# Performance work log

Hardware: AMD Instinct MI355X
Metric: run time of the kernel (lower is better)

The kernel has to match this reference:

```python
import jax, jax.numpy as jnp
import numpy as np

EMBED_DIM = 1024
NUM_HEADS = 16
HEAD_DIM = EMBED_DIM // NUM_HEADS
SCALE = HEAD_DIM ** -0.5


def setup_inputs() -> dict:
    key = jax.random.key(0)
    ks = jax.random.split(key, 9)
    B, N = 2, 2048
    s = EMBED_DIM ** -0.5  # ~ torch Linear init scale
    x = jax.random.normal(ks[0], (B, N, EMBED_DIM), dtype=jnp.float32)
    Wq = jax.random.uniform(ks[1], (EMBED_DIM, EMBED_DIM), jnp.float32, -s, s)
    bq = jax.random.uniform(ks[2], (EMBED_DIM,), jnp.float32, -s, s)
    Wk = jax.random.uniform(ks[3], (EMBED_DIM, EMBED_DIM), jnp.float32, -s, s)
    bk = jax.random.uniform(ks[4], (EMBED_DIM,), jnp.float32, -s, s)
    Wv = jax.random.uniform(ks[5], (EMBED_DIM, EMBED_DIM), jnp.float32, -s, s)
    bv = jax.random.uniform(ks[6], (EMBED_DIM,), jnp.float32, -s, s)
    Wo = jax.random.uniform(ks[7], (EMBED_DIM, EMBED_DIM), jnp.float32, -s, s)
    bo = jax.random.uniform(ks[8], (EMBED_DIM,), jnp.float32, -s, s)
    return {"x": x, "Wq": Wq, "bq": bq, "Wk": Wk, "bk": bk,
            "Wv": Wv, "bv": bv, "Wo": Wo, "bo": bo}


def reference(x, Wq, bq, Wk, bk, Wv, bv, Wo, bo):
    B, N, R = x.shape
    H, D = NUM_HEADS, HEAD_DIM
    # projections: Linear(x) = x @ W^T + b; reshape to (B, H, N, D)
    def proj(W, b):
        return (x @ W.T + b).reshape(B, N, H, D).transpose(0, 2, 1, 3)
    q = proj(Wq, bq)
    k = proj(Wk, bk)
    v = proj(Wv, bv)
    attn = jnp.einsum('bhnd,bhmd->bhnm', q, k) * SCALE  # (B,H,N,N)
    attn = jax.nn.softmax(attn, axis=-1)
    out = jnp.einsum('bhnm,bhmd->bhnd', attn, v)        # (B,H,N,D)
    out = out.transpose(0, 2, 1, 3).reshape(B, N, R)
    return out @ Wo.T + bo
```

## Files before the change

kernel.cpp:

```cpp
#include <hip/hip_runtime.h>
#include <stdint.h>

typedef __bf16 bf16;
typedef __bf16 bf16x4 __attribute__((ext_vector_type(4)));
typedef __bf16 bf16x8 __attribute__((ext_vector_type(8)));
typedef float f32x4 __attribute__((ext_vector_type(4)));

#define MFMA16(a, b, c) __builtin_amdgcn_mfma_f32_16x16x32_bf16((a), (b), (c), 0, 0, 0)

#define EMBED 1024
#define SEQ   2048
#define MROWS 4096
#define ATTN_QSCALE 0.1803368801111f

__device__ __forceinline__ void gl2lds16(const bf16* g, bf16* l) {
    __builtin_amdgcn_global_load_lds(
        (const __attribute__((address_space(1))) void*)g,
        (__attribute__((address_space(3))) void*)l,
        16, 0, 0);
}

__global__ __launch_bounds__(256) void cast_all_kernel(
    const float* __restrict__ x,  const float* __restrict__ Wq,
    const float* __restrict__ Wk, const float* __restrict__ Wv,
    const float* __restrict__ Wo, bf16* __restrict__ dst) {
    const int blk = blockIdx.x;
    const float* src;
    size_t so, dofs;
    if (blk < 2048) {
        src = x; so = (size_t)blk * 2048; dofs = so;
    } else {
        const int w = (blk - 2048) >> 9;
        so  = (size_t)((blk - 2048) & 511) * 2048;
        src = (w == 0) ? Wq : (w == 1) ? Wk : (w == 2) ? Wv : Wo;
        dofs = (size_t)(4 + w) * 1024 * 1024 + so;
    }
    const size_t i = (size_t)threadIdx.x * 8;
    float4 a = *(const float4*)(src + so + i);
    float4 b = *(const float4*)(src + so + i + 4);
    bf16x8 o;
    o[0] = (bf16)a.x; o[1] = (bf16)a.y; o[2] = (bf16)a.z; o[3] = (bf16)a.w;
    o[4] = (bf16)b.x; o[5] = (bf16)b.y; o[6] = (bf16)b.z; o[7] = (bf16)b.w;
    *(bf16x8*)(dst + dofs + i) = o;
}

template <bool SCALE>
__device__ __forceinline__ void gemm_tile(const bf16* __restrict__ A,
                                          const bf16* __restrict__ W,
                                          const float* __restrict__ bias,
                                          bf16* __restrict__ C,
                                          int m0, int n0, bf16* smem) {
    const int lane = threadIdx.x & 63;
    const int wv   = threadIdx.x >> 6;
    const int wm   = (wv >> 1) * 64;
    const int wn   = (wv & 1) * 64;
    const int fr   = lane & 15;
    const int quad = lane >> 4;
    const int srow = wv * 16 + (lane >> 2);
    const int swz  = ((lane & 3) ^ ((lane >> 2) & 3)) * 8;
    const int fcol = (quad ^ (fr & 3)) * 8;

    f32x4 acc[4][4];
#pragma unroll
    for (int mt = 0; mt < 4; ++mt)
#pragma unroll
        for (int nt = 0; nt < 4; ++nt)
            acc[mt][nt] = (f32x4){0.f, 0.f, 0.f, 0.f};

    auto stage = [&](int kt, int bb) {
        bf16* As = smem + bb * 8192;
        bf16* Bs = As + 4096;
        const int k0 = kt * 32;
#pragma unroll
        for (int c = 0; c < 2; ++c) {
            gl2lds16(A + (size_t)(m0 + c * 64 + srow) * 1024 + k0 + swz,
                     &As[(c * 64 + wv * 16) * 32]);
            gl2lds16(W + (size_t)(n0 + c * 64 + srow) * 1024 + k0 + swz,
                     &Bs[(c * 64 + wv * 16) * 32]);
        }
    };

    stage(0, 0);
    stage(1, 1);
#pragma unroll
    for (int kt = 0; kt < 32; ++kt) {
        if (kt < 31) asm volatile("s_waitcnt vmcnt(4)" ::: "memory");
        else         asm volatile("s_waitcnt vmcnt(0)" ::: "memory");
        __builtin_amdgcn_s_barrier();
        if (kt < 30) stage(kt + 2, (kt + 2) % 3);
        const bf16* As = smem + (kt % 3) * 8192;
        const bf16* Bs = As + 4096;
        bf16x8 af[4], bfr[4];
#pragma unroll
        for (int t = 0; t < 4; ++t) {
            af[t]  = *(const bf16x8*)&As[(wm + t * 16 + fr) * 32 + fcol];
            bfr[t] = *(const bf16x8*)&Bs[(wn + t * 16 + fr) * 32 + fcol];
        }
        __builtin_amdgcn_s_setprio(1);
#pragma unroll
        for (int mt = 0; mt < 4; ++mt)
#pragma unroll
            for (int nt = 0; nt < 4; ++nt)
                acc[mt][nt] = MFMA16(af[mt], bfr[nt], acc[mt][nt]);
        __builtin_amdgcn_s_setprio(0);
    }

    float bv[4];
#pragma unroll
    for (int nt = 0; nt < 4; ++nt)
        bv[nt] = bias[n0 + wn + nt * 16 + fr];
    const int row4 = quad * 4;
#pragma unroll
    for (int mt = 0; mt < 4; ++mt)
#pragma unroll
        for (int nt = 0; nt < 4; ++nt)
#pragma unroll
            for (int r = 0; r < 4; ++r) {
                int m = m0 + wm + mt * 16 + row4 + r;
                int n = n0 + wn + nt * 16 + fr;
                float v = acc[mt][nt][r] + bv[nt];
                if (SCALE) v *= ATTN_QSCALE;
                C[(size_t)m * 1024 + n] = (bf16)v;
            }
}

__device__ __forceinline__ void v_tile(const bf16* __restrict__ x,
                                       const bf16* __restrict__ Wv,
                                       const float* __restrict__ bias,
                                       bf16* __restrict__ VT,
                                       int m0, int n0, bf16* smem) {
    const int lane = threadIdx.x & 63;
    const int wv   = threadIdx.x >> 6;
    const int wmW  = (wv >> 1) * 64;
    const int wnT  = (wv & 1) * 64;
    const int f    = lane & 15;
    const int quad = lane >> 4;
    const int srow = wv * 16 + (lane >> 2);
    const int swz  = ((lane & 3) ^ ((lane >> 2) & 3)) * 8;
    const int fcol = (quad ^ (f & 3)) * 8;

    f32x4 acc[4][4];
#pragma unroll
    for (int mt = 0; mt < 4; ++mt)
#pragma unroll
        for (int nt = 0; nt < 4; ++nt)
            acc[mt][nt] = (f32x4){0.f, 0.f, 0.f, 0.f};

    auto stage = [&](int kt, int bb) {
        bf16* As = smem + bb * 8192;
        bf16* Bs = As + 4096;
        const int k0 = kt * 32;
#pragma unroll
        for (int c = 0; c < 2; ++c) {
            gl2lds16(x  + (size_t)(m0 + c * 64 + srow) * 1024 + k0 + swz,
                     &As[(c * 64 + wv * 16) * 32]);
            gl2lds16(Wv + (size_t)(n0 + c * 64 + srow) * 1024 + k0 + swz,
                     &Bs[(c * 64 + wv * 16) * 32]);
        }
    };

    stage(0, 0);
    stage(1, 1);
#pragma unroll
    for (int kt = 0; kt < 32; ++kt) {
        if (kt < 31) asm volatile("s_waitcnt vmcnt(4)" ::: "memory");
        else         asm volatile("s_waitcnt vmcnt(0)" ::: "memory");
        __builtin_amdgcn_s_barrier();
        if (kt < 30) stage(kt + 2, (kt + 2) % 3);
        const bf16* As = smem + (kt % 3) * 8192;
        const bf16* Bs = As + 4096;
        bf16x8 wf[4], xf[4];
#pragma unroll
        for (int t = 0; t < 4; ++t) {
            wf[t] = *(const bf16x8*)&Bs[(wmW + t * 16 + f) * 32 + fcol];
            xf[t] = *(const bf16x8*)&As[(wnT + t * 16 + f) * 32 + fcol];
        }
        __builtin_amdgcn_s_setprio(1);
#pragma unroll
        for (int mt = 0; mt < 4; ++mt)
#pragma unroll
            for (int nt = 0; nt < 4; ++nt)
                acc[mt][nt] = MFMA16(wf[mt], xf[nt], acc[mt][nt]);
        __builtin_amdgcn_s_setprio(0);
    }

    float4 b4[4];
#pragma unroll
    for (int mt = 0; mt < 4; ++mt)
        b4[mt] = *(const float4*)&bias[n0 + wmW + mt * 16 + quad * 4];

    __syncthreads();

#pragma unroll
    for (int mt = 0; mt < 4; ++mt)
#pragma unroll
        for (int nt = 0; nt < 4; ++nt) {
            const int tok = wnT + nt * 16 + f;
#pragma unroll
            for (int r = 0; r < 4; ++r) {
                const float bvr = (r == 0) ? b4[mt].x : (r == 1) ? b4[mt].y
                                : (r == 2) ? b4[mt].z : b4[mt].w;
                smem[(wmW + mt * 16 + quad * 4 + r) * 136 + tok] =
                    (bf16)(acc[mt][nt][r] + bvr);
            }
        }
    __syncthreads();

    const int n_r  = threadIdx.x >> 4;
    const int t8   = (threadIdx.x & 15) * 8;
    const int base = t8 & ~31;
    const int u4   = ((t8 >> 3) & 3) * 4;
    const int bb   = m0 >> 11;
    const int tokg = (m0 & 2047) + t8;
#pragma unroll
    for (int p = 0; p < 8; ++p) {
        const int n_loc = p * 16 + n_r;
        const bf16* row = &smem[n_loc * 136];
        bf16x4 a = *(const bf16x4*)&row[base + u4];
        bf16x4 b = *(const bf16x4*)&row[base + 16 + u4];
        bf16x8 v = {a[0], a[1], a[2], a[3], b[0], b[1], b[2], b[3]};
        *(bf16x8*)&VT[((size_t)(bb * 1024 + n0 + n_loc)) * 2048 + tokg] = v;
    }
}

__global__ __launch_bounds__(256) void qkv_kernel(
    const bf16* __restrict__ x,
    const bf16* __restrict__ Wq, const float* __restrict__ bq,
    const bf16* __restrict__ Wk, const float* __restrict__ bk,
    const bf16* __restrict__ Wv, const float* __restrict__ bv,
    bf16* __restrict__ Q, bf16* __restrict__ K, bf16* __restrict__ VT) {
    __shared__ __align__(16) bf16 smem[24576];
    const int m0    = blockIdx.x * 128;
    const int which = blockIdx.y >> 3;
    const int n0    = (blockIdx.y & 7) * 128;
    if (which == 0)      gemm_tile<true>(x, Wq, bq, Q, m0, n0, smem);
    else if (which == 1) gemm_tile<false>(x, Wk, bk, K, m0, n0, smem);
    else                 v_tile(x, Wv, bv, VT, m0, n0, smem);
}

__global__ __launch_bounds__(256) void oproj_kernel(
    const bf16* __restrict__ A, const bf16* __restrict__ W,
    const float* __restrict__ bias, float* __restrict__ C) {
    const int m0 = blockIdx.x * 128;
    const int n0 = blockIdx.y * 64;

    __shared__ __align__(16) bf16 smem[18432];

    const int lane = threadIdx.x & 63;
    const int wv   = threadIdx.x >> 6;
    const int wm   = (wv >> 1) * 64;
    const int wn   = (wv & 1) * 32;
    const int fr   = lane & 15;
    const int quad = lane >> 4;
    const int srow = wv * 16 + (lane >> 2);
    const int swz  = ((lane & 3) ^ ((lane >> 2) & 3)) * 8;
    const int fcol = (quad ^ (fr & 3)) * 8;

    f32x4 acc[4][2];
#pragma unroll
    for (int mt = 0; mt < 4; ++mt)
#pragma unroll
        for (int nt = 0; nt < 2; ++nt)
            acc[mt][nt] = (f32x4){0.f, 0.f, 0.f, 0.f};

    auto stage = [&](int kt, int bb) {
        bf16* As = smem + bb * 6144;
        bf16* Bs = As + 4096;
        const int k0 = kt * 32;
#pragma unroll
        for (int c = 0; c < 2; ++c)
            gl2lds16(A + (size_t)(m0 + c * 64 + srow) * 1024 + k0 + swz,
                     &As[(c * 64 + wv * 16) * 32]);
        gl2lds16(W + (size_t)(n0 + srow) * 1024 + k0 + swz,
                 &Bs[(wv * 16) * 32]);
    };

    stage(0, 0);
    stage(1, 1);
#pragma unroll
    for (int kt = 0; kt < 32; ++kt) {
        if (kt < 31) asm volatile("s_waitcnt vmcnt(3)" ::: "memory");
        else         asm volatile("s_waitcnt vmcnt(0)" ::: "memory");
        __builtin_amdgcn_s_barrier();
        if (kt < 30) stage(kt + 2, (kt + 2) % 3);
        const bf16* As = smem + (kt % 3) * 6144;
        const bf16* Bs = As + 4096;
        bf16x8 af[4], bfr[2];
#pragma unroll
        for (int t = 0; t < 4; ++t)
            af[t] = *(const bf16x8*)&As[(wm + t * 16 + fr) * 32 + fcol];
#pragma unroll
        for (int t = 0; t < 2; ++t)
            bfr[t] = *(const bf16x8*)&Bs[(wn + t * 16 + fr) * 32 + fcol];
        __builtin_amdgcn_s_setprio(1);
#pragma unroll
        for (int mt = 0; mt < 4; ++mt)
#pragma unroll
            for (int nt = 0; nt < 2; ++nt)
                acc[mt][nt] = MFMA16(af[mt], bfr[nt], acc[mt][nt]);
        __builtin_amdgcn_s_setprio(0);
    }

    float bv[2];
#pragma unroll
    for (int nt = 0; nt < 2; ++nt)
        bv[nt] = bias[n0 + wn + nt * 16 + fr];
    const int row4 = quad * 4;
#pragma unroll
    for (int mt = 0; mt < 4; ++mt)
#pragma unroll
        for (int nt = 0; nt < 2; ++nt)
#pragma unroll
            for (int r = 0; r < 4; ++r) {
                int m = m0 + wm + mt * 16 + row4 + r;
                int n = n0 + wn + nt * 16 + fr;
                C[(size_t)m * 1024 + n] = acc[mt][nt][r] + bv[nt];
            }
}

__global__ __launch_bounds__(256, 2) void attn_kernel(
    const bf16* __restrict__ Q, const bf16* __restrict__ K,
    const bf16* __restrict__ VT, bf16* __restrict__ Opart,
    float* __restrict__ lpart) {
    const int tid  = threadIdx.x;
    const int lane = tid & 63;
    const int wv   = tid >> 6;
    const int quad = lane >> 4;
    const int f    = lane & 15;
    const int lin  = blockIdx.y * 16 + blockIdx.x;
    const int sw   = (lin & 7) * 64 + (lin >> 3);
    const int qh   = sw & 15;
    const int bh   = sw >> 4;
    const int qt   = qh >> 1;
    const int half = qh & 1;
    const int q0   = qt * 256;
    const int kvb  = half * 1024;
    const int b    = bh >> 4;
    const int h    = bh & 15;

    const bf16* Qp = Q + ((size_t)b * SEQ) * 1024 + (size_t)h * 64;
    const bf16* Kp = K + ((size_t)b * SEQ) * 1024 + (size_t)h * 64;
    const bf16* Vp = VT + ((size_t)(b * 1024 + h * 64)) * 2048;
    bf16*  Op = Opart + (size_t)half * MROWS * 1024
                      + ((size_t)b * SEQ) * 1024 + (size_t)h * 64;
    float* lp = lpart + ((size_t)(half * 2 + b) * 16 + h) * SEQ;

    __shared__ bf16 Ks[4][64 * 64];
    __shared__ bf16 VTs[4][64 * 64];

    bf16x8 qf[4][2];
#pragma unroll
    for (int qg = 0; qg < 4; ++qg) {
        const bf16* qrow = Qp + (size_t)(q0 + wv * 64 + qg * 16 + f) * 1024;
        qf[qg][0] = *(const bf16x8*)(qrow + quad * 8);
        qf[qg][1] = *(const bf16x8*)(qrow + 32 + quad * 8);
    }

    const int srow = wv * 8 + (lane >> 3);
    const int swz  = (((lane & 7) ^ ((lane >> 3) & 7))) * 8;
    auto stageK = [&](int t, int bb) {
        const int kv0 = kvb + t * 64;
#pragma unroll
        for (int i = 0; i < 2; ++i)
            gl2lds16(Kp + (size_t)(kv0 + i * 32 + srow) * 1024 + swz,
                     &Ks[bb][(i * 32 + wv * 8) * 64]);
    };
    auto stageVT = [&](int t, int bb) {
        const int kv0 = kvb + t * 64;
#pragma unroll
        for (int i = 0; i < 2; ++i)
            gl2lds16(Vp + (size_t)(i * 32 + srow) * 2048 + kv0 + swz,
                     &VTs[bb][(i * 32 + wv * 8) * 64]);
    };

    stageK(0, 0); stageVT(0, 0);
    stageK(1, 1); stageVT(1, 1);

    f32x4 oacc[4][4];
#pragma unroll
    for (int qg = 0; qg < 4; ++qg)
#pragma unroll
        for (int t = 0; t < 4; ++t)
            oacc[qg][t] = (f32x4){0.f, 0.f, 0.f, 0.f};
    f32x4 lacc[4];
#pragma unroll
    for (int qg = 0; qg < 4; ++qg)
        lacc[qg] = (f32x4){0.f, 0.f, 0.f, 0.f};
    const bf16x8 ones8 = {(bf16)1.f, (bf16)1.f, (bf16)1.f, (bf16)1.f,
                          (bf16)1.f, (bf16)1.f, (bf16)1.f, (bf16)1.f};
    const f32x4  zero4 = (f32x4){0.f, 0.f, 0.f, 0.f};

    const int fcol0 = (quad ^ (f & 7)) * 8;
    const int fcol1 = ((4 + quad) ^ (f & 7)) * 8;

    bf16x8 pbA[4][2], pbB[4][2];

    asm volatile("s_waitcnt vmcnt(4)" ::: "memory");
    __builtin_amdgcn_s_barrier();
    {
        bf16x8 kf0[4], kf1[4];
#pragma unroll
        for (int t4 = 0; t4 < 4; ++t4) {
            kf0[t4] = *(const bf16x8*)&Ks[0][(t4 * 16 + f) * 64 + fcol0];
            kf1[t4] = *(const bf16x8*)&Ks[0][(t4 * 16 + f) * 64 + fcol1];
        }
#pragma unroll
        for (int qg = 0; qg < 4; ++qg) {
            f32x4 s[4];
            __builtin_amdgcn_s_setprio(1);
#pragma unroll
            for (int t4 = 0; t4 < 4; ++t4) {
                s[t4] = MFMA16(kf0[t4], qf[qg][0], zero4);
                s[t4] = MFMA16(kf1[t4], qf[qg][1], s[t4]);
            }
            __builtin_amdgcn_s_setprio(0);
#pragma unroll
            for (int kt = 0; kt < 2; ++kt) {
#pragma unroll
                for (int r = 0; r < 4; ++r) {
                    pbA[qg][kt][r]     = (bf16)__builtin_amdgcn_exp2f(s[2 * kt][r]);
                    pbA[qg][kt][4 + r] = (bf16)__builtin_amdgcn_exp2f(s[2 * kt + 1][r]);
                }
                lacc[qg] = MFMA16(ones8, pbA[qg][kt], lacc[qg]);
            }
        }
    }

    auto step = [&](int t, bf16x8 (&pbc)[4][2], bf16x8 (&pbn)[4][2],
                    int drain, bool doStage, bool doQK) {
        if (doStage) { stageK(t + 2, (t + 2) & 3); stageVT(t + 2, (t + 2) & 3); }
        if (drain == 4) asm volatile("s_waitcnt vmcnt(4)" ::: "memory");
        else            asm volatile("s_waitcnt vmcnt(0)" ::: "memory");
        __builtin_amdgcn_s_barrier();
        const int bq = (t + 1) & 3;
        const int bp = t & 3;

        bf16x8 kf0[4], kf1[4];
        if (doQK) {
#pragma unroll
            for (int t4 = 0; t4 < 4; ++t4) {
                kf0[t4] = *(const bf16x8*)&Ks[bq][(t4 * 16 + f) * 64 + fcol0];
                kf1[t4] = *(const bf16x8*)&Ks[bq][(t4 * 16 + f) * 64 + fcol1];
            }
        }
#pragma unroll
        for (int u = 0; u < 4; ++u) {
            f32x4 s[4];
            if (doQK) {
                __builtin_amdgcn_s_setprio(1);
#pragma unroll
                for (int t4 = 0; t4 < 4; ++t4) {
                    s[t4] = MFMA16(kf0[t4], qf[u][0], zero4);
                    s[t4] = MFMA16(kf1[t4], qf[u][1], s[t4]);
                }
                __builtin_amdgcn_s_setprio(0);
            }
            __builtin_amdgcn_s_setprio(1);
#pragma unroll
            for (int kt = 0; kt < 2; ++kt) {
                const int pc = ((kt * 4 + quad) ^ (f & 7)) * 8;
                bf16x8 vf = *(const bf16x8*)&VTs[bp][(u * 16 + f) * 64 + pc];
#pragma unroll
                for (int qg = 0; qg < 4; ++qg)
                    oacc[qg][u] = MFMA16(vf, pbc[qg][kt], oacc[qg][u]);
            }
            __builtin_amdgcn_s_setprio(0);
            if (doQK) {
#pragma unroll
                for (int kt = 0; kt < 2; ++kt) {
#pragma unroll
                    for (int r = 0; r < 4; ++r) {
                        pbn[u][kt][r]     = (bf16)__builtin_amdgcn_exp2f(s[2 * kt][r]);
                        pbn[u][kt][4 + r] = (bf16)__builtin_amdgcn_exp2f(s[2 * kt + 1][r]);
                    }
                    lacc[u] = MFMA16(ones8, pbn[u][kt], lacc[u]);
                }
            }
        }
    };

    for (int tt = 0; tt < 14; tt += 2) {
        step(tt,     pbA, pbB, 4, true, true);
        step(tt + 1, pbB, pbA, 4, true, true);
    }
    step(14, pbA, pbB, 0, false, true);
    step(15, pbB, pbA, 0, false, false);

#pragma unroll
    for (int qg = 0; qg < 4; ++qg) {
        const int q = q0 + wv * 64 + qg * 16 + f;
        bf16* orow = Op + (size_t)q * 1024;
#pragma unroll
        for (int dt = 0; dt < 4; ++dt) {
            bf16x4 ov;
#pragma unroll
            for (int r = 0; r < 4; ++r)
                ov[r] = (bf16)oacc[qg][dt][r];
            *(bf16x4*)(orow + dt * 16 + quad * 4) = ov;
        }
        if (quad == 0)
            lp[q] = lacc[qg][0];
    }
}

__global__ __launch_bounds__(256) void combine_kernel(
    const bf16* __restrict__ Opart, const float* __restrict__ lpart,
    bf16* __restrict__ O) {
    const int gid = blockIdx.x * 256 + threadIdx.x;
    const int row = gid >> 7;
    const int c8  = (gid & 127) * 8;
    const int b   = row >> 11;
    const int tok = row & 2047;
    const int h   = c8 >> 6;

    const float l = lpart[((size_t)(0 * 2 + b) * 16 + h) * SEQ + tok]
                  + lpart[((size_t)(1 * 2 + b) * 16 + h) * SEQ + tok];
    const float inv = 1.0f / l;

    const size_t off = (size_t)row * 1024 + c8;
    bf16x8 a = *(const bf16x8*)&Opart[off];
    bf16x8 c = *(const bf16x8*)&Opart[(size_t)MROWS * 1024 + off];
    bf16x8 o;
#pragma unroll
    for (int i = 0; i < 8; ++i)
        o[i] = (bf16)(((float)a[i] + (float)c[i]) * inv);
    *(bf16x8*)&O[off] = o;
}

extern "C" void kernel_launch(void* const* d_in, const int* in_sizes, int n_in,
                              void* d_out, int out_size, void* d_ws, size_t ws_size,
                              hipStream_t stream) {
    const float* x  = (const float*)d_in[0];
    const float* Wq = (const float*)d_in[1];
    const float* bq = (const float*)d_in[2];
    const float* Wk = (const float*)d_in[3];
    const float* bk = (const float*)d_in[4];
    const float* Wv = (const float*)d_in[5];
    const float* bv = (const float*)d_in[6];
    const float* Wo = (const float*)d_in[7];
    const float* bo = (const float*)d_in[8];
    float* out = (float*)d_out;

    bf16* xb    = (bf16*)d_ws;
    bf16* Wqb   = xb   + (size_t)MROWS * 1024;
    bf16* Wkb   = Wqb  + (size_t)1024 * 1024;
    bf16* Wvb   = Wkb  + (size_t)1024 * 1024;
    bf16* Wob   = Wvb  + (size_t)1024 * 1024;
    bf16* Q     = Wob  + (size_t)1024 * 1024;
    bf16* K     = Q    + (size_t)MROWS * 1024;
    bf16* VT    = K    + (size_t)MROWS * 1024;
    bf16* O     = VT   + (size_t)MROWS * 1024;
    bf16* Opart = O    + (size_t)MROWS * 1024;
    float* lpart = (float*)(Opart + (size_t)2 * MROWS * 1024);

    cast_all_kernel<<<4096, 256, 0, stream>>>(x, Wq, Wk, Wv, Wo, xb);

    qkv_kernel<<<dim3(32, 24), 256, 0, stream>>>(xb, Wqb, bq, Wkb, bk, Wvb, bv, Q, K, VT);
    attn_kernel<<<dim3(16, 32), 256, 0, stream>>>(Q, K, VT, Opart, lpart);
    combine_kernel<<<2048, 256, 0, stream>>>(Opart, lpart, O);
    oproj_kernel<<<dim3(32, 16), 256, 0, stream>>>(O, Wob, bo, out);
}
```

Baseline: 180.0 us.

## Drop KV split in attention, shrink query tile, remove combine kernel; retune LDS swizzle

The attention kernel no longer splits the KV range into two halves with a separate combine pass. Each block now handles 128 queries over the full 2048-key range and normalizes by the row sum before storing O directly. This removes the partial-output write/read traffic and a kernel launch, but halves per-wave query reuse of each K/V tile and doubles the loop length per block. Separately, the GEMM LDS swizzles gain an extra XOR term, aimed at reducing bank conflicts in the projection kernels.

```diff
diff --git a/kernel.cpp b/kernel.cpp
--- a/kernel.cpp
+++ b/kernel.cpp
@@ -57,8 +57,8 @@
     const int fr   = lane & 15;
     const int quad = lane >> 4;
     const int srow = wv * 16 + (lane >> 2);
-    const int swz  = ((lane & 3) ^ ((lane >> 2) & 3)) * 8;
-    const int fcol = (quad ^ (fr & 3)) * 8;
+    const int swz  = ((lane & 3) ^ ((lane >> 2) & 3) ^ ((lane >> 4) & 3)) * 8;
+    const int fcol = (quad ^ (fr & 3) ^ (fr >> 2)) * 8;
 
     f32x4 acc[4][4];
 #pragma unroll
@@ -136,8 +136,8 @@
     const int f    = lane & 15;
     const int quad = lane >> 4;
     const int srow = wv * 16 + (lane >> 2);
-    const int swz  = ((lane & 3) ^ ((lane >> 2) & 3)) * 8;
-    const int fcol = (quad ^ (f & 3)) * 8;
+    const int swz  = ((lane & 3) ^ ((lane >> 2) & 3) ^ ((lane >> 4) & 3)) * 8;
+    const int fcol = (quad ^ (f & 3) ^ (f >> 2)) * 8;
 
     f32x4 acc[4][4];
 #pragma unroll
@@ -253,8 +253,8 @@
     const int fr   = lane & 15;
     const int quad = lane >> 4;
     const int srow = wv * 16 + (lane >> 2);
-    const int swz  = ((lane & 3) ^ ((lane >> 2) & 3)) * 8;
-    const int fcol = (quad ^ (fr & 3)) * 8;
+    const int swz  = ((lane & 3) ^ ((lane >> 2) & 3) ^ ((lane >> 4) & 3)) * 8;
+    const int fcol = (quad ^ (fr & 3) ^ (fr >> 2)) * 8;
 
     f32x4 acc[4][2];
 #pragma unroll
@@ -320,8 +320,7 @@
 
 __global__ __launch_bounds__(256, 2) void attn_kernel(
     const bf16* __restrict__ Q, const bf16* __restrict__ K,
-    const bf16* __restrict__ VT, bf16* __restrict__ Opart,
-    float* __restrict__ lpart) {
+    const bf16* __restrict__ VT, bf16* __restrict__ O) {
     const int tid  = threadIdx.x;
     const int lane = tid & 63;
     const int wv   = tid >> 6;
@@ -329,29 +328,24 @@
     const int f    = lane & 15;
     const int lin  = blockIdx.y * 16 + blockIdx.x;
     const int sw   = (lin & 7) * 64 + (lin >> 3);
-    const int qh   = sw & 15;
+    const int qt   = sw & 15;
     const int bh   = sw >> 4;
-    const int qt   = qh >> 1;
-    const int half = qh & 1;
-    const int q0   = qt * 256;
-    const int kvb  = half * 1024;
+    const int q0   = qt * 128;
     const int b    = bh >> 4;
     const int h    = bh & 15;
 
     const bf16* Qp = Q + ((size_t)b * SEQ) * 1024 + (size_t)h * 64;
     const bf16* Kp = K + ((size_t)b * SEQ) * 1024 + (size_t)h * 64;
     const bf16* Vp = VT + ((size_t)(b * 1024 + h * 64)) * 2048;
-    bf16*  Op = Opart + (size_t)half * MROWS * 1024
-                      + ((size_t)b * SEQ) * 1024 + (size_t)h * 64;
-    float* lp = lpart + ((size_t)(half * 2 + b) * 16 + h) * SEQ;
+    bf16* Op = O + ((size_t)b * SEQ) * 1024 + (size_t)h * 64;
 
     __shared__ bf16 Ks[4][64 * 64];
     __shared__ bf16 VTs[4][64 * 64];
 
-    bf16x8 qf[4][2];
-#pragma unroll
-    for (int qg = 0; qg < 4; ++qg) {
-        const bf16* qrow = Qp + (size_t)(q0 + wv * 64 + qg * 16 + f) * 1024;
+    bf16x8 qf[2][2];
+#pragma unroll
+    for (int qg = 0; qg < 2; ++qg) {
+        const bf16* qrow = Qp + (size_t)(q0 + wv * 32 + qg * 16 + f) * 1024;
         qf[qg][0] = *(const bf16x8*)(qrow + quad * 8);
         qf[qg][1] = *(const bf16x8*)(qrow + 32 + quad * 8);
     }
@@ -359,14 +353,14 @@
     const int srow = wv * 8 + (lane >> 3);
     const int swz  = (((lane & 7) ^ ((lane >> 3) & 7))) * 8;
     auto stageK = [&](int t, int bb) {
-        const int kv0 = kvb + t * 64;
+        const int kv0 = t * 64;
 #pragma unroll
         for (int i = 0; i < 2; ++i)
             gl2lds16(Kp + (size_t)(kv0 + i * 32 + srow) * 1024 + swz,
                      &Ks[bb][(i * 32 + wv * 8) * 64]);
     };
     auto stageVT = [&](int t, int bb) {
-        const int kv0 = kvb + t * 64;
+        const int kv0 = t * 64;
 #pragma unroll
         for (int i = 0; i < 2; ++i)
             gl2lds16(Vp + (size_t)(i * 32 + srow) * 2048 + kv0 + swz,
@@ -376,15 +370,15 @@
     stageK(0, 0); stageVT(0, 0);
     stageK(1, 1); stageVT(1, 1);
 
-    f32x4 oacc[4][4];
-#pragma unroll
-    for (int qg = 0; qg < 4; ++qg)
+    f32x4 oacc[2][4];
+#pragma unroll
+    for (int qg = 0; qg < 2; ++qg)
 #pragma unroll
         for (int t = 0; t < 4; ++t)
             oacc[qg][t] = (f32x4){0.f, 0.f, 0.f, 0.f};
-    f32x4 lacc[4];
-#pragma unroll
-    for (int qg = 0; qg < 4; ++qg)
+    f32x4 lacc[2];
+#pragma unroll
+    for (int qg = 0; qg < 2; ++qg)
         lacc[qg] = (f32x4){0.f, 0.f, 0.f, 0.f};
     const bf16x8 ones8 = {(bf16)1.f, (bf16)1.f, (bf16)1.f, (bf16)1.f,
                           (bf16)1.f, (bf16)1.f, (bf16)1.f, (bf16)1.f};
@@ -393,7 +387,7 @@
     const int fcol0 = (quad ^ (f & 7)) * 8;
     const int fcol1 = ((4 + quad) ^ (f & 7)) * 8;
 
-    bf16x8 pbA[4][2], pbB[4][2];
+    bf16x8 pbA[2][2], pbB[2][2];
 
     asm volatile("s_waitcnt vmcnt(4)" ::: "memory");
     __builtin_amdgcn_s_barrier();
@@ -405,7 +399,7 @@
             kf1[t4] = *(const bf16x8*)&Ks[0][(t4 * 16 + f) * 64 + fcol1];
         }
 #pragma unroll
-        for (int qg = 0; qg < 4; ++qg) {
+        for (int qg = 0; qg < 2; ++qg) {
             f32x4 s[4];
             __builtin_amdgcn_s_setprio(1);
 #pragma unroll
@@ -426,7 +420,7 @@
         }
     }
 
-    auto step = [&](int t, bf16x8 (&pbc)[4][2], bf16x8 (&pbn)[4][2],
+    auto step = [&](int t, bf16x8 (&pbc)[2][2], bf16x8 (&pbn)[2][2],
                     int drain, bool doStage, bool doQK) {
         if (doStage) { stageK(t + 2, (t + 2) & 3); stageVT(t + 2, (t + 2) & 3); }
         if (drain == 4) asm volatile("s_waitcnt vmcnt(4)" ::: "memory");
@@ -446,7 +440,8 @@
 #pragma unroll
         for (int u = 0; u < 4; ++u) {
             f32x4 s[4];
-            if (doQK) {
+            const bool qk = doQK && u < 2;
+            if (qk) {
                 __builtin_amdgcn_s_setprio(1);
 #pragma unroll
                 for (int t4 = 0; t4 < 4; ++t4) {
@@ -461,11 +456,11 @@
                 const int pc = ((kt * 4 + quad) ^ (f & 7)) * 8;
                 bf16x8 vf = *(const bf16x8*)&VTs[bp][(u * 16 + f) * 64 + pc];
 #pragma unroll
-                for (int qg = 0; qg < 4; ++qg)
+                for (int qg = 0; qg < 2; ++qg)
                     oacc[qg][u] = MFMA16(vf, pbc[qg][kt], oacc[qg][u]);
             }
             __builtin_amdgcn_s_setprio(0);
-            if (doQK) {
+            if (qk) {
 #pragma unroll
                 for (int kt = 0; kt < 2; ++kt) {
 #pragma unroll
@@ -479,52 +474,27 @@
         }
     };
 
-    for (int tt = 0; tt < 14; tt += 2) {
+    for (int tt = 0; tt < 30; tt += 2) {
         step(tt,     pbA, pbB, 4, true, true);
         step(tt + 1, pbB, pbA, 4, true, true);
     }
-    step(14, pbA, pbB, 0, false, true);
-    step(15, pbB, pbA, 0, false, false);
-
-#pragma unroll
-    for (int qg = 0; qg < 4; ++qg) {
-        const int q = q0 + wv * 64 + qg * 16 + f;
+    step(30, pbA, pbB, 0, false, true);
+    step(31, pbB, pbA, 0, false, false);
+
+#pragma unroll
+    for (int qg = 0; qg < 2; ++qg) {
+        const float inv = 1.0f / lacc[qg][0];
+        const int q = q0 + wv * 32 + qg * 16 + f;
         bf16* orow = Op + (size_t)q * 1024;
 #pragma unroll
         for (int dt = 0; dt < 4; ++dt) {
             bf16x4 ov;
 #pragma unroll
             for (int r = 0; r < 4; ++r)
-                ov[r] = (bf16)oacc[qg][dt][r];
+                ov[r] = (bf16)(oacc[qg][dt][r] * inv);
             *(bf16x4*)(orow + dt * 16 + quad * 4) = ov;
         }
-        if (quad == 0)
-            lp[q] = lacc[qg][0];
-    }
-}
-
-__global__ __launch_bounds__(256) void combine_kernel(
-    const bf16* __restrict__ Opart, const float* __restrict__ lpart,
-    bf16* __restrict__ O) {
-    const int gid = blockIdx.x * 256 + threadIdx.x;
-    const int row = gid >> 7;
-    const int c8  = (gid & 127) * 8;
-    const int b   = row >> 11;
-    const int tok = row & 2047;
-    const int h   = c8 >> 6;
-
-    const float l = lpart[((size_t)(0 * 2 + b) * 16 + h) * SEQ + tok]
-                  + lpart[((size_t)(1 * 2 + b) * 16 + h) * SEQ + tok];
-    const float inv = 1.0f / l;
-
-    const size_t off = (size_t)row * 1024 + c8;
-    bf16x8 a = *(const bf16x8*)&Opart[off];
-    bf16x8 c = *(const bf16x8*)&Opart[(size_t)MROWS * 1024 + off];
-    bf16x8 o;
-#pragma unroll
-    for (int i = 0; i < 8; ++i)
-        o[i] = (bf16)(((float)a[i] + (float)c[i]) * inv);
-    *(bf16x8*)&O[off] = o;
+    }
 }
 
 extern "C" void kernel_launch(void* const* d_in, const int* in_sizes, int n_in,
@@ -550,13 +520,10 @@
     bf16* K     = Q    + (size_t)MROWS * 1024;
     bf16* VT    = K    + (size_t)MROWS * 1024;
     bf16* O     = VT   + (size_t)MROWS * 1024;
-    bf16* Opart = O    + (size_t)MROWS * 1024;
-    float* lpart = (float*)(Opart + (size_t)2 * MROWS * 1024);
 
     cast_all_kernel<<<4096, 256, 0, stream>>>(x, Wq, Wk, Wv, Wo, xb);
 
     qkv_kernel<<<dim3(32, 24), 256, 0, stream>>>(xb, Wqb, bq, Wkb, bk, Wvb, bv, Q, K, VT);
-    attn_kernel<<<dim3(16, 32), 256, 0, stream>>>(Q, K, VT, Opart, lpart);
-    combine_kernel<<<2048, 256, 0, stream>>>(Opart, lpart, O);
+    attn_kernel<<<dim3(16, 32), 256, 0, stream>>>(Q, K, VT, O);
     oproj_kernel<<<dim3(32, 16), 256, 0, stream>>>(O, Wob, bo, out);
 }
```

New measurement: 175.1 us, median of 2. 1.03x faster.
